# Optimization experiments

Measured on AMD Instinct MI355X. Metric: run time of the kernel, lower is better.

Reference implementation:

```python
import jax, jax.numpy as jnp
import numpy as np

N_NODES = 50000
N_EDGES = 800000
IN_DIM = 128
HID = 256
B_SEEDS = 8192
EPS = 1e-12


def _sage_layer(h, src, dst, Wn, Ws, b):
    # mean-aggregation SAGEConv: fc_self(h) + fc_neigh(mean over in-neighbors)
    msgs = h[src]  # [E, d]
    agg = jax.ops.segment_sum(msgs, dst, num_segments=N_NODES)
    cnt = jax.ops.segment_sum(jnp.ones((src.shape[0], 1), h.dtype), dst, num_segments=N_NODES)
    neigh = agg / jnp.maximum(cnt, 1.0)
    return neigh @ Wn + h @ Ws + b


def _sage(x, src, dst, Wn1, Ws1, b1, Wn2, Ws2, b2):
    h = jax.nn.relu(_sage_layer(x, src, dst, Wn1, Ws1, b1))
    return _sage_layer(h, src, dst, Wn2, Ws2, b2)


def _l2norm(x):
    # F.normalize(p=2, dim=1)
    n = jnp.sqrt(jnp.sum(x * x, axis=1, keepdims=True))
    return x / jnp.maximum(n, EPS)


def _unique_gather(h, ids):
    # torch.unique(ids, return_inverse=True) then h[inverse]
    uniq, inv = jnp.unique(ids, return_inverse=True, size=ids.shape[0], fill_value=0)
    return h[uniq][inv]


def setup_inputs() -> dict:
    key = jax.random.key(0)
    ks = jax.random.split(key, 16)
    s = lambda d: 1.0 / np.sqrt(d)
    return {
        "x_i": jax.random.normal(ks[0], (N_NODES, IN_DIM), jnp.float32),
        "x_j": jax.random.normal(ks[1], (N_NODES, IN_DIM), jnp.float32),
        "src_i": jax.random.randint(ks[2], (N_EDGES,), 0, N_NODES, jnp.int32),
        "dst_i": jax.random.randint(ks[3], (N_EDGES,), 0, N_NODES, jnp.int32),
        "src_j": jax.random.randint(ks[4], (N_EDGES,), 0, N_NODES, jnp.int32),
        "dst_j": jax.random.randint(ks[5], (N_EDGES,), 0, N_NODES, jnp.int32),
        "ids_i": jax.random.randint(ks[6], (B_SEEDS,), 0, N_NODES, jnp.int32),
        "ids_j": jax.random.randint(ks[7], (B_SEEDS,), 0, N_NODES, jnp.int32),
        "Wn1": jax.random.normal(ks[8], (IN_DIM, HID), jnp.float32) * s(IN_DIM),
        "Ws1": jax.random.normal(ks[9], (IN_DIM, HID), jnp.float32) * s(IN_DIM),
        "b1": jnp.zeros((HID,), jnp.float32),
        "Wn2": jax.random.normal(ks[10], (HID, HID), jnp.float32) * s(HID),
        "Ws2": jax.random.normal(ks[11], (HID, HID), jnp.float32) * s(HID),
        "b2": jnp.zeros((HID,), jnp.float32),
        "W_out": jax.random.normal(ks[12], (2 * HID, 1), jnp.float32) * s(2 * HID),
        "b_out": jnp.zeros((1,), jnp.float32),
    }


def reference(x_i, x_j, src_i, dst_i, src_j, dst_j, ids_i, ids_j,
              Wn1, Ws1, b1, Wn2, Ws2, b2, W_out, b_out):
    sage_o_i = _l2norm(_sage(x_i, src_i, dst_i, Wn1, Ws1, b1, Wn2, Ws2, b2))
    sage_o_j = _l2norm(_sage(x_j, src_j, dst_j, Wn1, Ws1, b1, Wn2, Ws2, b2))
    g_i = _unique_gather(sage_o_i, ids_i)  # [B, HID]
    g_j = _unique_gather(sage_o_j, ids_j)
    h_cur = jnp.concatenate([g_i, g_j], axis=-1) @ W_out + b_out  # [B, 1]
    return jnp.stack([h_cur.squeeze(-1)])  # [1, B]
```

## Files before the change

kernel.cpp:

```cpp
#include <hip/hip_runtime.h>

constexpr int NN = 50000;
constexpr int NE = 800000;
constexpr int IND = 128;
constexpr int HD = 256;
constexpr int BS = 8192;
constexpr int NPAD = 50176;
constexpr int NBKT = 196;
constexpr int BCAP = 8192;

typedef __attribute__((ext_vector_type(8))) short short8v;
typedef __attribute__((ext_vector_type(4))) float floatx4;

__device__ inline ushort f2b(float f) {
  unsigned u = __float_as_uint(f);
  unsigned r = (u + 0x7fffu + ((u >> 16) & 1u)) >> 16;
  return (ushort)r;
}
__device__ inline float b2f(ushort b) {
  return __uint_as_float((unsigned)b << 16);
}
__device__ __forceinline__ void acc2(unsigned u, float& a0, float& a1) {
  a0 += __uint_as_float(u << 16);
  a1 += __uint_as_float(u & 0xffff0000u);
}
__device__ inline int wave_incl_scan(int x, int lane) {
#pragma unroll
  for (int d = 1; d < 64; d <<= 1) {
    int y = __shfl_up(x, d);
    if (lane >= d) x += y;
  }
  return x;
}

__device__ __forceinline__ void gload16(const ushort* g, ushort* l) {
  __builtin_amdgcn_global_load_lds(
      (const __attribute__((address_space(1))) void*)g,
      (__attribute__((address_space(3))) void*)l, 16, 0, 0);
}

__global__ __launch_bounds__(256) void k_prep(const float* __restrict__ Wn1,
                                              const float* __restrict__ Ws1,
                                              const float* __restrict__ Wn2,
                                              const float* __restrict__ Ws2,
                                              ushort* __restrict__ Wt,
                                              ushort* __restrict__ Whi,
                                              ushort* __restrict__ Wlo,
                                              int* __restrict__ bcnt) {
  const int b = blockIdx.x, t = threadIdx.x;
  if (b < 256) {
    int i = b * 256 + t;
    int n = i >> 8, k = i & 255;
    float v = (k < 128) ? Wn1[k * HD + n] : Ws1[(k - 128) * HD + n];
    Wt[n * 256 + k] = f2b(v);
  } else if (b < 768) {
    int i = (b - 256) * 256 + t;
    int n = i >> 9, k = i & 511;
    float v = (k < 256) ? Wn2[k * HD + n] : Ws2[(k - 256) * HD + n];
    ushort hi = f2b(v);
    Whi[n * 512 + k] = hi;
    Wlo[n * 512 + k] = f2b(v - b2f(hi));
  } else {
    for (int i = t; i < 2 * NBKT; i += 256) bcnt[i] = 0;
  }
}

__global__ __launch_bounds__(256) void k_bin(const int* __restrict__ src_i,
                                             const int* __restrict__ dst_i,
                                             const int* __restrict__ src_j,
                                             const int* __restrict__ dst_j,
                                             int* __restrict__ bcnt,
                                             int* __restrict__ bucketbuf) {
  __shared__ int hist[NBKT], gbase[NBKT], lcur[NBKT];
  const int blk = blockIdx.x;
  const int g = blk >= 98;
  const int c = blk - g * 98;
  const int* src = g ? src_j : src_i;
  const int* dst = g ? dst_j : dst_i;
  const int t = threadIdx.x;
  if (t < NBKT) hist[t] = 0;
  __syncthreads();
  const int e0 = c * 8192;
#pragma unroll
  for (int k = 0; k < 32; ++k) {
    int e = e0 + k * 256 + t;
    if (e < NE) atomicAdd(&hist[dst[e] >> 8], 1);
  }
  __syncthreads();
  if (t < NBKT) {
    int h = hist[t];
    gbase[t] = h ? atomicAdd(&bcnt[g * NBKT + t], h) : 0;
    lcur[t] = 0;
  }
  __syncthreads();
#pragma unroll
  for (int k = 0; k < 32; ++k) {
    int e = e0 + k * 256 + t;
    if (e < NE) {
      int d = dst[e];
      int b = d >> 8;
      int p = gbase[b] + atomicAdd(&lcur[b], 1);
      if (p < BCAP)
        bucketbuf[(g * NBKT + b) * BCAP + p] = (src[e] << 8) | (d & 255);
    }
  }
}

__global__ __launch_bounds__(256) void k_bktscan(const int* __restrict__ bcnt,
                                                 int* __restrict__ bktbase) {
  __shared__ int wt[4];
  __shared__ int carry, tot;
  const int t = threadIdx.x, lane = t & 63;
  if (t == 0) carry = 0;
  __syncthreads();
  for (int ch = 0; ch < 2; ++ch) {
    int i = ch * 256 + t;
    int v = (i < 2 * NBKT) ? min(bcnt[i], BCAP) : 0;
    int x = wave_incl_scan(v, lane);
    if (lane == 63) wt[t >> 6] = x;
    __syncthreads();
    if (t == 0) {
      int run = 0;
#pragma unroll
      for (int j = 0; j < 4; ++j) { int tv = wt[j]; wt[j] = run; run += tv; }
      tot = run;
    }
    __syncthreads();
    if (i < 2 * NBKT) bktbase[i] = carry + x - v + wt[t >> 6];
    __syncthreads();
    if (t == 0) carry += tot;
    __syncthreads();
  }
}

__global__ __launch_bounds__(256) void k_build(const int* __restrict__ bucketbuf,
                                               const int* __restrict__ bcnt,
                                               const int* __restrict__ bktbase,
                                               int* __restrict__ csr,
                                               int* __restrict__ cnt2,
                                               int* __restrict__ row_start2) {
  __shared__ int hist[256], lstart[256], lcur[256];
  __shared__ int stage[BCAP];
  __shared__ int wt[4];
  const int b = blockIdx.x;
  const int g = b >= NBKT;
  const int bb = b - g * NBKT;
  const int t = threadIdx.x, lane = t & 63;
  const int C = min(bcnt[b], BCAP);
  const int base = bktbase[b];
  const int* buf = bucketbuf + b * BCAP;
  hist[t] = 0;
  __syncthreads();
  for (int i = t; i < C; i += 256) atomicAdd(&hist[buf[i] & 255], 1);
  __syncthreads();
  int v = hist[t];
  int x = wave_incl_scan(v, lane);
  if (lane == 63) wt[t >> 6] = x;
  __syncthreads();
  if (t == 0) {
    int run = 0;
#pragma unroll
    for (int j = 0; j < 4; ++j) { int tv = wt[j]; wt[j] = run; run += tv; }
  }
  __syncthreads();
  int ls = x - v + wt[t >> 6];
  lstart[t] = ls;
  lcur[t] = ls;
  __syncthreads();
  for (int i = t; i < C; i += 256) {
    int val = buf[i];
    int p = atomicAdd(&lcur[val & 255], 1);
    stage[p] = val >> 8;
  }
  __syncthreads();
  for (int i = t; i < C; i += 256) csr[base + i] = stage[i];
  int node = bb * 256 + t;
  cnt2[g * NPAD + node] = v;
  row_start2[g * NPAD + node] = base + ls;
}

__global__ __launch_bounds__(256) void k_tobf16(const float* __restrict__ x_i,
                                                const float* __restrict__ x_j,
                                                ushort* __restrict__ xb2) {
  int i = blockIdx.x * 256 + threadIdx.x;
  int e4 = i * 4;
  int g = e4 >= NN * IND;
  const float* xp = g ? x_j : x_i;
  float4 v = *(const float4*)(xp + (e4 - g * NN * IND));
  ushort4 u;
  u.x = f2b(v.x); u.y = f2b(v.y); u.z = f2b(v.z); u.w = f2b(v.w);
  *(ushort4*)(xb2 + e4) = u;
}

__global__ __launch_bounds__(256) void k_agg1(const ushort* __restrict__ xb2,
                                              const int* __restrict__ csr,
                                              const int* __restrict__ row_start2,
                                              const int* __restrict__ cnt2,
                                              ushort* __restrict__ aggb2) {
  int w = threadIdx.x >> 6, l = threadIdx.x & 63;
  int p = blockIdx.x * 4 + w;
  int nA = p * 2;
  int g = nA >= NN;
  int nl = nA - g * NN;
  int base = g * NPAD + nl;
  int stA = row_start2[base], degA = cnt2[base];
  int stB = row_start2[base + 1], degB = cnt2[base + 1];
  const ushort* xb = xb2 + g * NN * IND;
  float a0A = 0.f, a1A = 0.f, a0B = 0.f, a1B = 0.f;
  int cmn = min(degA, degB);
  int e = 0;
  for (; e + 4 <= cmn; e += 4) {
    int sA0 = csr[stA + e + 0], sA1 = csr[stA + e + 1];
    int sA2 = csr[stA + e + 2], sA3 = csr[stA + e + 3];
    int sB0 = csr[stB + e + 0], sB1 = csr[stB + e + 1];
    int sB2 = csr[stB + e + 2], sB3 = csr[stB + e + 3];
    unsigned uA0 = *(const unsigned*)(xb + sA0 * IND + 2 * l);
    unsigned uA1 = *(const unsigned*)(xb + sA1 * IND + 2 * l);
    unsigned uA2 = *(const unsigned*)(xb + sA2 * IND + 2 * l);
    unsigned uA3 = *(const unsigned*)(xb + sA3 * IND + 2 * l);
    unsigned uB0 = *(const unsigned*)(xb + sB0 * IND + 2 * l);
    unsigned uB1 = *(const unsigned*)(xb + sB1 * IND + 2 * l);
    unsigned uB2 = *(const unsigned*)(xb + sB2 * IND + 2 * l);
    unsigned uB3 = *(const unsigned*)(xb + sB3 * IND + 2 * l);
    acc2(uA0, a0A, a1A); acc2(uA1, a0A, a1A);
    acc2(uA2, a0A, a1A); acc2(uA3, a0A, a1A);
    acc2(uB0, a0B, a1B); acc2(uB1, a0B, a1B);
    acc2(uB2, a0B, a1B); acc2(uB3, a0B, a1B);
  }
  int eA = e, eB = e;
  for (; eA + 4 <= degA; eA += 4) {
    int s0 = csr[stA + eA + 0], s1 = csr[stA + eA + 1];
    int s2 = csr[stA + eA + 2], s3 = csr[stA + eA + 3];
    unsigned u0 = *(const unsigned*)(xb + s0 * IND + 2 * l);
    unsigned u1 = *(const unsigned*)(xb + s1 * IND + 2 * l);
    unsigned u2 = *(const unsigned*)(xb + s2 * IND + 2 * l);
    unsigned u3 = *(const unsigned*)(xb + s3 * IND + 2 * l);
    acc2(u0, a0A, a1A); acc2(u1, a0A, a1A);
    acc2(u2, a0A, a1A); acc2(u3, a0A, a1A);
  }
  for (; eA < degA; ++eA) {
    int s = csr[stA + eA];
    unsigned u = *(const unsigned*)(xb + s * IND + 2 * l);
    acc2(u, a0A, a1A);
  }
  for (; eB + 4 <= degB; eB += 4) {
    int s0 = csr[stB + eB + 0], s1 = csr[stB + eB + 1];
    int s2 = csr[stB + eB + 2], s3 = csr[stB + eB + 3];
    unsigned u0 = *(const unsigned*)(xb + s0 * IND + 2 * l);
    unsigned u1 = *(const unsigned*)(xb + s1 * IND + 2 * l);
    unsigned u2 = *(const unsigned*)(xb + s2 * IND + 2 * l);
    unsigned u3 = *(const unsigned*)(xb + s3 * IND + 2 * l);
    acc2(u0, a0B, a1B); acc2(u1, a0B, a1B);
    acc2(u2, a0B, a1B); acc2(u3, a0B, a1B);
  }
  for (; eB < degB; ++eB) {
    int s = csr[stB + eB];
    unsigned u = *(const unsigned*)(xb + s * IND + 2 * l);
    acc2(u, a0B, a1B);
  }
  float invA = 1.f / (float)max(degA, 1);
  float invB = 1.f / (float)max(degB, 1);
  ushort2 uA, uB;
  uA.x = f2b(a0A * invA); uA.y = f2b(a1A * invA);
  uB.x = f2b(a0B * invB); uB.y = f2b(a1B * invB);
  *(ushort2*)(aggb2 + (g * NN + nl) * IND + 2 * l) = uA;
  *(ushort2*)(aggb2 + (g * NN + nl + 1) * IND + 2 * l) = uB;
}

__global__ __launch_bounds__(256) void k_gemm1(const ushort* __restrict__ aggb2,
                                               const ushort* __restrict__ xb2,
                                               const ushort* __restrict__ Wt,
                                               const float* __restrict__ b1,
                                               ushort* __restrict__ h1b2) {
  __shared__ ushort smem[16384];
  const int t = threadIdx.x;
  const int g = blockIdx.x >= 392;
  const int row0 = (blockIdx.x - g * 392) * 128, col0 = blockIdx.y * 128;
  const ushort* aggb = aggb2 + g * NN * IND;
  const ushort* xb = xb2 + g * NN * IND;
  ushort* h1b = h1b2 + g * NN * HD;
  const int w = t >> 6, l = t & 63;
  const int wm = w & 1, wn = w >> 1;

  const int r0 = t >> 2, cs0 = t & 3;
  const int c0 = cs0 ^ (r0 & 3);
  const int rA0 = min(row0 + r0, NN - 1);
  const int rA1 = min(row0 + r0 + 64, NN - 1);
  const int gA0 = rA0 * IND + c0 * 8;
  const int gA1 = rA1 * IND + c0 * 8;
  const int gB0 = (col0 + r0) * 256 + c0 * 8;
  const int gB1 = (col0 + r0 + 64) * 256 + c0 * 8;
  const int wofs = w * 512;

  floatx4 acc[4][4];
#pragma unroll
  for (int i = 0; i < 4; ++i)
#pragma unroll
    for (int j = 0; j < 4; ++j) acc[i][j] = (floatx4){0.f, 0.f, 0.f, 0.f};

#define STAGE(buf, kk)                                                      \
  do {                                                                      \
    const ushort* Ab = ((kk) < 128) ? (aggb + (kk)) : (xb + ((kk) - 128));  \
    ushort* Ald = smem + (buf) * 4096;                                      \
    ushort* Bld = smem + 8192 + (buf) * 4096;                               \
    gload16(Ab + gA0, Ald + wofs);                                          \
    gload16(Ab + gA1, Ald + 2048 + wofs);                                   \
    gload16(Wt + gB0 + (kk), Bld + wofs);                                   \
    gload16(Wt + gB1 + (kk), Bld + 2048 + wofs);                            \
  } while (0)

  STAGE(0, 0);
  __syncthreads();
  int cur = 0;
  const int rA = l & 15, gg = l >> 4;
  for (int step = 0; step < 8; ++step) {
    if (step < 7) STAGE(cur ^ 1, (step + 1) * 32);
    const ushort* Abuf = smem + cur * 4096;
    const ushort* Bbuf = smem + 8192 + cur * 4096;
    short8v af[4], bf[4];
#pragma unroll
    for (int i = 0; i < 4; ++i) {
      int r = wm * 64 + i * 16 + rA;
      af[i] = *(const short8v*)(Abuf + r * 32 + ((gg ^ (r & 3)) * 8));
    }
#pragma unroll
    for (int j = 0; j < 4; ++j) {
      int r = wn * 64 + j * 16 + rA;
      bf[j] = *(const short8v*)(Bbuf + r * 32 + ((gg ^ (r & 3)) * 8));
    }
#pragma unroll
    for (int i = 0; i < 4; ++i)
#pragma unroll
      for (int j = 0; j < 4; ++j)
        acc[i][j] = __builtin_amdgcn_mfma_f32_16x16x32_bf16(af[i], bf[j],
                                                            acc[i][j], 0, 0, 0);
    if (step < 7) {
      __syncthreads();
      cur ^= 1;
    }
  }
#undef STAGE

  __syncthreads();
  const int rD = l >> 4, cD = l & 15;
#pragma unroll
  for (int j = 0; j < 4; ++j) {
    int cl = wn * 64 + j * 16 + cD;
    float bias = b1[col0 + cl];
#pragma unroll
    for (int i = 0; i < 4; ++i) {
      int rbase = wm * 64 + i * 16 + rD * 4;
#pragma unroll
      for (int rr = 0; rr < 4; ++rr)
        smem[(rbase + rr) * 128 + cl] = f2b(fmaxf(acc[i][j][rr] + bias, 0.f));
    }
  }
  __syncthreads();
  const int rl = t >> 4, ch = t & 15;
#pragma unroll
  for (int it = 0; it < 8; ++it) {
    int row_l = rl + it * 16;
    int grow = row0 + row_l;
    if (grow < NN)
      *(short8v*)(h1b + grow * HD + col0 + ch * 8) =
          *(const short8v*)(smem + row_l * 128 + ch * 8);
  }
}

__global__ __launch_bounds__(256) void k_agg2(
    const ushort* __restrict__ h1b2, const int* __restrict__ csr,
    const int* __restrict__ row_start2, const int* __restrict__ cnt2,
    const int* __restrict__ ids_i, const int* __restrict__ ids_j,
    ushort* __restrict__ A2) {
  __shared__ float red[4][HD];
  const int b = blockIdx.x;
  const int g = b >= BS;
  const int node = (g ? ids_j : ids_i)[b - g * BS];
  const int st = row_start2[g * NPAD + node], deg = cnt2[g * NPAD + node];
  const ushort* h1b = h1b2 + g * NN * HD;
  const int w = threadIdx.x >> 6, l = threadIdx.x & 63;
  float a0 = 0.f, a1 = 0.f, a2 = 0.f, a3 = 0.f;
  int e = w;
  for (; e + 4 < deg; e += 8) {
    int sa = csr[st + e], sb = csr[st + e + 4];
    uint2 ua = *(const uint2*)(h1b + sa * HD + l * 4);
    uint2 ub = *(const uint2*)(h1b + sb * HD + l * 4);
    acc2(ua.x, a0, a1); acc2(ua.y, a2, a3);
    acc2(ub.x, a0, a1); acc2(ub.y, a2, a3);
  }
  if (e < deg) {
    int sa = csr[st + e];
    uint2 ua = *(const uint2*)(h1b + sa * HD + l * 4);
    acc2(ua.x, a0, a1); acc2(ua.y, a2, a3);
  }
  red[w][l * 4 + 0] = a0;
  red[w][l * 4 + 1] = a1;
  red[w][l * 4 + 2] = a2;
  red[w][l * 4 + 3] = a3;
  __syncthreads();
  const int t = threadIdx.x;
  float s = (red[0][t] + red[1][t]) + (red[2][t] + red[3][t]);
  s *= 1.f / (float)max(deg, 1);
  A2[b * 512 + t] = f2b(s);
  A2[b * 512 + 256 + t] = h1b[node * HD + t];
}

__global__ __launch_bounds__(256) void k_head(const ushort* __restrict__ A2,
                                              const ushort* __restrict__ Whi,
                                              const ushort* __restrict__ Wlo,
                                              const float* __restrict__ b2,
                                              const float* __restrict__ W_out,
                                              float* __restrict__ outP) {
  __shared__ ushort Ahl[64 * 32];
  __shared__ ushort Bhl[256 * 32];
  __shared__ ushort Bll[256 * 32];
  __shared__ float sred[4][64][2];
  const int t = threadIdx.x;
  const int row0 = blockIdx.x * 64;
  const int w = t >> 6, l = t & 63;
  const int woff = (row0 >= BS) ? 256 : 0;
  floatx4 acc[4][4];
#pragma unroll
  for (int i = 0; i < 4; ++i)
#pragma unroll
    for (int j = 0; j < 4; ++j) acc[i][j] = (floatx4){0.f, 0.f, 0.f, 0.f};

  for (int kk = 0; kk < 512; kk += 32) {
    {
      int r = t >> 2, c = t & 3;
      int sw = (c ^ (r & 3)) * 8;
      *(short8v*)(Ahl + r * 32 + sw) =
          *(const short8v*)(A2 + (row0 + r) * 512 + kk + c * 8);
    }
#pragma unroll
    for (int s = t; s < 1024; s += 256) {
      int r = s >> 2, c = s & 3;
      int sw = (c ^ (r & 3)) * 8;
      *(short8v*)(Bhl + r * 32 + sw) =
          *(const short8v*)(Whi + r * 512 + kk + c * 8);
      *(short8v*)(Bll + r * 32 + sw) =
          *(const short8v*)(Wlo + r * 512 + kk + c * 8);
    }
    __syncthreads();
    const int rA = l & 15, gg = l >> 4;
    short8v af[4], bh[4], bl[4];
#pragma unroll
    for (int i = 0; i < 4; ++i) {
      int r = i * 16 + rA;
      af[i] = *(const short8v*)(Ahl + r * 32 + ((gg ^ (r & 3)) * 8));
    }
#pragma unroll
    for (int j = 0; j < 4; ++j) {
      int r = w * 64 + j * 16 + rA;
      int sw = (gg ^ (r & 3)) * 8;
      bh[j] = *(const short8v*)(Bhl + r * 32 + sw);
      bl[j] = *(const short8v*)(Bll + r * 32 + sw);
    }
#pragma unroll
    for (int i = 0; i < 4; ++i)
#pragma unroll
      for (int j = 0; j < 4; ++j) {
        acc[i][j] = __builtin_amdgcn_mfma_f32_16x16x32_bf16(af[i], bh[j],
                                                            acc[i][j], 0, 0, 0);
        acc[i][j] = __builtin_amdgcn_mfma_f32_16x16x32_bf16(af[i], bl[j],
                                                            acc[i][j], 0, 0, 0);
      }
    __syncthreads();
  }
  const int cD = l & 15, rD = l >> 4;
  float bj[4], wo[4];
#pragma unroll
  for (int j = 0; j < 4; ++j) {
    int col = w * 64 + j * 16 + cD;
    bj[j] = b2[col];
    wo[j] = W_out[woff + col];
  }
#pragma unroll
  for (int i = 0; i < 4; ++i)
#pragma unroll
    for (int rr = 0; rr < 4; ++rr) {
      float ssv = 0.f, dpv = 0.f;
#pragma unroll
      for (int j = 0; j < 4; ++j) {
        float v = acc[i][j][rr] + bj[j];
        ssv += v * v;
        dpv += v * wo[j];
      }
#pragma unroll
      for (int d = 1; d < 16; d <<= 1) {
        ssv += __shfl_xor(ssv, d);
        dpv += __shfl_xor(dpv, d);
      }
      if (cD == 0) {
        int row = i * 16 + rD * 4 + rr;
        sred[w][row][0] = ssv;
        sred[w][row][1] = dpv;
      }
    }
  __syncthreads();
  if (t < 64) {
    float ss = (sred[0][t][0] + sred[1][t][0]) + (sred[2][t][0] + sred[3][t][0]);
    float dp = (sred[0][t][1] + sred[1][t][1]) + (sred[2][t][1] + sred[3][t][1]);
    outP[row0 + t] = dp / fmaxf(sqrtf(ss), 1e-12f);
  }
}

__global__ __launch_bounds__(256) void k_out2(const float* __restrict__ outP,
                                              const float* __restrict__ b_out,
                                              float* __restrict__ out) {
  int s = blockIdx.x * 256 + threadIdx.x;
  if (s < BS) out[s] = outP[s] + outP[s + BS] + b_out[0];
}

extern "C" void kernel_launch(void* const* d_in, const int* in_sizes, int n_in,
                              void* d_out, int out_size, void* d_ws,
                              size_t ws_size, hipStream_t stream) {
  (void)in_sizes; (void)n_in; (void)out_size; (void)ws_size;
  const float* x_i = (const float*)d_in[0];
  const float* x_j = (const float*)d_in[1];
  const int* src_i = (const int*)d_in[2];
  const int* dst_i = (const int*)d_in[3];
  const int* src_j = (const int*)d_in[4];
  const int* dst_j = (const int*)d_in[5];
  const int* ids_i = (const int*)d_in[6];
  const int* ids_j = (const int*)d_in[7];
  const float* Wn1 = (const float*)d_in[8];
  const float* Ws1 = (const float*)d_in[9];
  const float* b1 = (const float*)d_in[10];
  const float* Wn2 = (const float*)d_in[11];
  const float* Ws2 = (const float*)d_in[12];
  const float* b2 = (const float*)d_in[13];
  const float* W_out = (const float*)d_in[14];
  const float* b_out = (const float*)d_in[15];
  float* out = (float*)d_out;

  char* w = (char*)d_ws;
  int* bcnt       = (int*)(w + 0);
  int* bktbase    = (int*)(w + 2048);
  int* cnt2       = (int*)(w + 4096);
  int* row_start2 = (int*)(w + 405504);
  int* bucketbuf  = (int*)(w + 806912);
  ushort* Wt      = (ushort*)(w + 13651968);
  ushort* W2hi    = (ushort*)(w + 13783040);
  ushort* W2lo    = (ushort*)(w + 14045184);
  ushort* xb2     = (ushort*)(w + 14307328);
  ushort* aggb2   = (ushort*)(w + 39907328);
  ushort* h1b2    = (ushort*)(w + 65507328);
  int* csr        = (int*)(w + 116707328);
  ushort* A2      = (ushort*)(w + 14307328);
  float* outP     = (float*)(w + 31084544);

  k_prep<<<769, 256, 0, stream>>>(Wn1, Ws1, Wn2, Ws2, Wt, W2hi, W2lo, bcnt);
  k_bin<<<196, 256, 0, stream>>>(src_i, dst_i, src_j, dst_j, bcnt, bucketbuf);
  k_bktscan<<<1, 256, 0, stream>>>(bcnt, bktbase);
  k_build<<<392, 256, 0, stream>>>(bucketbuf, bcnt, bktbase, csr, cnt2,
                                   row_start2);
  k_tobf16<<<12500, 256, 0, stream>>>(x_i, x_j, xb2);
  k_agg1<<<12500, 256, 0, stream>>>(xb2, csr, row_start2, cnt2, aggb2);
  k_gemm1<<<dim3(784, 2), 256, 0, stream>>>(aggb2, xb2, Wt, b1, h1b2);
  k_agg2<<<2 * BS, 256, 0, stream>>>(h1b2, csr, row_start2, cnt2, ids_i, ids_j,
                                     A2);
  k_head<<<256, 256, 0, stream>>>(A2, W2hi, W2lo, b2, W_out, outP);
  k_out2<<<32, 256, 0, stream>>>(outP, b_out, out);
}
```

Baseline: 211.8 us.

## Fuse prep, binning and bf16 conversion; fold bucket scan into build; widen gathers

Weight conversion, edge binning and feature bf16 conversion now run as one kernel launch. The bucket counter reset becomes a memset, and the one-block bucket scan is recomputed redundantly inside each build block, so two launches go away. The layer-1 aggregation now uses one wave per node, with half-waves taking alternate edges and 8-byte loads. The layer-2 aggregation uses 16-byte loads with half-wave splitting and shuffle reductions. The aim is lower launch overhead and better memory-level parallelism, at the cost of the same scan being repeated in every build block.

```diff
diff --git a/kernel.cpp b/kernel.cpp
--- a/kernel.cpp
+++ b/kernel.cpp
@@ -39,45 +39,49 @@
       (__attribute__((address_space(3))) void*)l, 16, 0, 0);
 }
 
-__global__ __launch_bounds__(256) void k_prep(const float* __restrict__ Wn1,
-                                              const float* __restrict__ Ws1,
-                                              const float* __restrict__ Wn2,
-                                              const float* __restrict__ Ws2,
-                                              ushort* __restrict__ Wt,
-                                              ushort* __restrict__ Whi,
-                                              ushort* __restrict__ Wlo,
-                                              int* __restrict__ bcnt) {
+__global__ __launch_bounds__(256) void k_bin_cvt(
+    const float* __restrict__ Wn1, const float* __restrict__ Ws1,
+    const float* __restrict__ Wn2, const float* __restrict__ Ws2,
+    ushort* __restrict__ Wt, ushort* __restrict__ Whi,
+    ushort* __restrict__ Wlo, const int* __restrict__ src_i,
+    const int* __restrict__ dst_i, const int* __restrict__ src_j,
+    const int* __restrict__ dst_j, int* __restrict__ bcnt,
+    int* __restrict__ bucketbuf, const float* __restrict__ x_i,
+    const float* __restrict__ x_j, ushort* __restrict__ xb2) {
+  __shared__ int hist[NBKT], gbase[NBKT], lcur[NBKT];
   const int b = blockIdx.x, t = threadIdx.x;
   if (b < 256) {
     int i = b * 256 + t;
     int n = i >> 8, k = i & 255;
     float v = (k < 128) ? Wn1[k * HD + n] : Ws1[(k - 128) * HD + n];
     Wt[n * 256 + k] = f2b(v);
-  } else if (b < 768) {
+    return;
+  }
+  if (b < 768) {
     int i = (b - 256) * 256 + t;
     int n = i >> 9, k = i & 511;
     float v = (k < 256) ? Wn2[k * HD + n] : Ws2[(k - 256) * HD + n];
     ushort hi = f2b(v);
     Whi[n * 512 + k] = hi;
     Wlo[n * 512 + k] = f2b(v - b2f(hi));
-  } else {
-    for (int i = t; i < 2 * NBKT; i += 256) bcnt[i] = 0;
-  }
-}
-
-__global__ __launch_bounds__(256) void k_bin(const int* __restrict__ src_i,
-                                             const int* __restrict__ dst_i,
-                                             const int* __restrict__ src_j,
-                                             const int* __restrict__ dst_j,
-                                             int* __restrict__ bcnt,
-                                             int* __restrict__ bucketbuf) {
-  __shared__ int hist[NBKT], gbase[NBKT], lcur[NBKT];
-  const int blk = blockIdx.x;
+    return;
+  }
+  if (b >= 964) {
+    int i = (b - 964) * 256 + t;
+    int e4 = i * 4;
+    int g = e4 >= NN * IND;
+    const float* xp = g ? x_j : x_i;
+    float4 v = *(const float4*)(xp + (e4 - g * NN * IND));
+    ushort4 u;
+    u.x = f2b(v.x); u.y = f2b(v.y); u.z = f2b(v.z); u.w = f2b(v.w);
+    *(ushort4*)(xb2 + e4) = u;
+    return;
+  }
+  const int blk = b - 768;
   const int g = blk >= 98;
   const int c = blk - g * 98;
   const int* src = g ? src_j : src_i;
   const int* dst = g ? dst_j : dst_i;
-  const int t = threadIdx.x;
   if (t < NBKT) hist[t] = 0;
   __syncthreads();
   const int e0 = c * 8192;
@@ -98,18 +102,26 @@
     int e = e0 + k * 256 + t;
     if (e < NE) {
       int d = dst[e];
-      int b = d >> 8;
-      int p = gbase[b] + atomicAdd(&lcur[b], 1);
+      int bk = d >> 8;
+      int p = gbase[bk] + atomicAdd(&lcur[bk], 1);
       if (p < BCAP)
-        bucketbuf[(g * NBKT + b) * BCAP + p] = (src[e] << 8) | (d & 255);
-    }
-  }
-}
-
-__global__ __launch_bounds__(256) void k_bktscan(const int* __restrict__ bcnt,
-                                                 int* __restrict__ bktbase) {
-  __shared__ int wt[4];
-  __shared__ int carry, tot;
+        bucketbuf[(g * NBKT + bk) * BCAP + p] = (src[e] << 8) | (d & 255);
+    }
+  }
+}
+
+__global__ __launch_bounds__(256) void k_build(const int* __restrict__ bucketbuf,
+                                               const int* __restrict__ bcnt,
+                                               int* __restrict__ csr,
+                                               int* __restrict__ cnt2,
+                                               int* __restrict__ row_start2) {
+  __shared__ int hist[256], lcur[256];
+  __shared__ int stage[BCAP];
+  __shared__ int wtv[4];
+  __shared__ int carry, tot, baseSh;
+  const int b = blockIdx.x;
+  const int g = b >= NBKT;
+  const int bb = b - g * NBKT;
   const int t = threadIdx.x, lane = t & 63;
   if (t == 0) carry = 0;
   __syncthreads();
@@ -117,37 +129,22 @@
     int i = ch * 256 + t;
     int v = (i < 2 * NBKT) ? min(bcnt[i], BCAP) : 0;
     int x = wave_incl_scan(v, lane);
-    if (lane == 63) wt[t >> 6] = x;
+    if (lane == 63) wtv[t >> 6] = x;
     __syncthreads();
     if (t == 0) {
       int run = 0;
 #pragma unroll
-      for (int j = 0; j < 4; ++j) { int tv = wt[j]; wt[j] = run; run += tv; }
+      for (int j = 0; j < 4; ++j) { int tv = wtv[j]; wtv[j] = run; run += tv; }
       tot = run;
     }
     __syncthreads();
-    if (i < 2 * NBKT) bktbase[i] = carry + x - v + wt[t >> 6];
+    if (i == b) baseSh = carry + x - v + wtv[t >> 6];
     __syncthreads();
     if (t == 0) carry += tot;
     __syncthreads();
   }
-}
-
-__global__ __launch_bounds__(256) void k_build(const int* __restrict__ bucketbuf,
-                                               const int* __restrict__ bcnt,
-                                               const int* __restrict__ bktbase,
-                                               int* __restrict__ csr,
-                                               int* __restrict__ cnt2,
-                                               int* __restrict__ row_start2) {
-  __shared__ int hist[256], lstart[256], lcur[256];
-  __shared__ int stage[BCAP];
-  __shared__ int wt[4];
-  const int b = blockIdx.x;
-  const int g = b >= NBKT;
-  const int bb = b - g * NBKT;
-  const int t = threadIdx.x, lane = t & 63;
+  const int base = baseSh;
   const int C = min(bcnt[b], BCAP);
-  const int base = bktbase[b];
   const int* buf = bucketbuf + b * BCAP;
   hist[t] = 0;
   __syncthreads();
@@ -155,16 +152,15 @@
   __syncthreads();
   int v = hist[t];
   int x = wave_incl_scan(v, lane);
-  if (lane == 63) wt[t >> 6] = x;
+  if (lane == 63) wtv[t >> 6] = x;
   __syncthreads();
   if (t == 0) {
     int run = 0;
 #pragma unroll
-    for (int j = 0; j < 4; ++j) { int tv = wt[j]; wt[j] = run; run += tv; }
-  }
-  __syncthreads();
-  int ls = x - v + wt[t >> 6];
-  lstart[t] = ls;
+    for (int j = 0; j < 4; ++j) { int tv = wtv[j]; wtv[j] = run; run += tv; }
+  }
+  __syncthreads();
+  int ls = x - v + wtv[t >> 6];
   lcur[t] = ls;
   __syncthreads();
   for (int i = t; i < C; i += 256) {
@@ -177,19 +173,6 @@
   int node = bb * 256 + t;
   cnt2[g * NPAD + node] = v;
   row_start2[g * NPAD + node] = base + ls;
-}
-
-__global__ __launch_bounds__(256) void k_tobf16(const float* __restrict__ x_i,
-                                                const float* __restrict__ x_j,
-                                                ushort* __restrict__ xb2) {
-  int i = blockIdx.x * 256 + threadIdx.x;
-  int e4 = i * 4;
-  int g = e4 >= NN * IND;
-  const float* xp = g ? x_j : x_i;
-  float4 v = *(const float4*)(xp + (e4 - g * NN * IND));
-  ushort4 u;
-  u.x = f2b(v.x); u.y = f2b(v.y); u.z = f2b(v.z); u.w = f2b(v.w);
-  *(ushort4*)(xb2 + e4) = u;
 }
 
 __global__ __launch_bounds__(256) void k_agg1(const ushort* __restrict__ xb2,
@@ -198,73 +181,49 @@
                                               const int* __restrict__ cnt2,
                                               ushort* __restrict__ aggb2) {
   int w = threadIdx.x >> 6, l = threadIdx.x & 63;
-  int p = blockIdx.x * 4 + w;
-  int nA = p * 2;
-  int g = nA >= NN;
-  int nl = nA - g * NN;
-  int base = g * NPAD + nl;
-  int stA = row_start2[base], degA = cnt2[base];
-  int stB = row_start2[base + 1], degB = cnt2[base + 1];
+  int n = blockIdx.x * 4 + w;
+  int g = n >= NN;
+  int nl = n - g * NN;
+  int st = row_start2[g * NPAD + nl], deg = cnt2[g * NPAD + nl];
   const ushort* xb = xb2 + g * NN * IND;
-  float a0A = 0.f, a1A = 0.f, a0B = 0.f, a1B = 0.f;
-  int cmn = min(degA, degB);
+  const int h = l >> 5, c = l & 31;
+  float a0 = 0.f, a1 = 0.f, a2 = 0.f, a3 = 0.f;
   int e = 0;
-  for (; e + 4 <= cmn; e += 4) {
-    int sA0 = csr[stA + e + 0], sA1 = csr[stA + e + 1];
-    int sA2 = csr[stA + e + 2], sA3 = csr[stA + e + 3];
-    int sB0 = csr[stB + e + 0], sB1 = csr[stB + e + 1];
-    int sB2 = csr[stB + e + 2], sB3 = csr[stB + e + 3];
-    unsigned uA0 = *(const unsigned*)(xb + sA0 * IND + 2 * l);
-    unsigned uA1 = *(const unsigned*)(xb + sA1 * IND + 2 * l);
-    unsigned uA2 = *(const unsigned*)(xb + sA2 * IND + 2 * l);
-    unsigned uA3 = *(const unsigned*)(xb + sA3 * IND + 2 * l);
-    unsigned uB0 = *(const unsigned*)(xb + sB0 * IND + 2 * l);
-    unsigned uB1 = *(const unsigned*)(xb + sB1 * IND + 2 * l);
-    unsigned uB2 = *(const unsigned*)(xb + sB2 * IND + 2 * l);
-    unsigned uB3 = *(const unsigned*)(xb + sB3 * IND + 2 * l);
-    acc2(uA0, a0A, a1A); acc2(uA1, a0A, a1A);
-    acc2(uA2, a0A, a1A); acc2(uA3, a0A, a1A);
-    acc2(uB0, a0B, a1B); acc2(uB1, a0B, a1B);
-    acc2(uB2, a0B, a1B); acc2(uB3, a0B, a1B);
-  }
-  int eA = e, eB = e;
-  for (; eA + 4 <= degA; eA += 4) {
-    int s0 = csr[stA + eA + 0], s1 = csr[stA + eA + 1];
-    int s2 = csr[stA + eA + 2], s3 = csr[stA + eA + 3];
-    unsigned u0 = *(const unsigned*)(xb + s0 * IND + 2 * l);
-    unsigned u1 = *(const unsigned*)(xb + s1 * IND + 2 * l);
-    unsigned u2 = *(const unsigned*)(xb + s2 * IND + 2 * l);
-    unsigned u3 = *(const unsigned*)(xb + s3 * IND + 2 * l);
-    acc2(u0, a0A, a1A); acc2(u1, a0A, a1A);
-    acc2(u2, a0A, a1A); acc2(u3, a0A, a1A);
-  }
-  for (; eA < degA; ++eA) {
-    int s = csr[stA + eA];
-    unsigned u = *(const unsigned*)(xb + s * IND + 2 * l);
-    acc2(u, a0A, a1A);
-  }
-  for (; eB + 4 <= degB; eB += 4) {
-    int s0 = csr[stB + eB + 0], s1 = csr[stB + eB + 1];
-    int s2 = csr[stB + eB + 2], s3 = csr[stB + eB + 3];
-    unsigned u0 = *(const unsigned*)(xb + s0 * IND + 2 * l);
-    unsigned u1 = *(const unsigned*)(xb + s1 * IND + 2 * l);
-    unsigned u2 = *(const unsigned*)(xb + s2 * IND + 2 * l);
-    unsigned u3 = *(const unsigned*)(xb + s3 * IND + 2 * l);
-    acc2(u0, a0B, a1B); acc2(u1, a0B, a1B);
-    acc2(u2, a0B, a1B); acc2(u3, a0B, a1B);
-  }
-  for (; eB < degB; ++eB) {
-    int s = csr[stB + eB];
-    unsigned u = *(const unsigned*)(xb + s * IND + 2 * l);
-    acc2(u, a0B, a1B);
-  }
-  float invA = 1.f / (float)max(degA, 1);
-  float invB = 1.f / (float)max(degB, 1);
-  ushort2 uA, uB;
-  uA.x = f2b(a0A * invA); uA.y = f2b(a1A * invA);
-  uB.x = f2b(a0B * invB); uB.y = f2b(a1B * invB);
-  *(ushort2*)(aggb2 + (g * NN + nl) * IND + 2 * l) = uA;
-  *(ushort2*)(aggb2 + (g * NN + nl + 1) * IND + 2 * l) = uB;
+  for (; e + 8 <= deg; e += 8) {
+    int s0 = csr[st + e + 0 + h];
+    int s1 = csr[st + e + 2 + h];
+    int s2 = csr[st + e + 4 + h];
+    int s3 = csr[st + e + 6 + h];
+    uint2 u0 = *(const uint2*)(xb + s0 * IND + c * 4);
+    uint2 u1 = *(const uint2*)(xb + s1 * IND + c * 4);
+    uint2 u2 = *(const uint2*)(xb + s2 * IND + c * 4);
+    uint2 u3 = *(const uint2*)(xb + s3 * IND + c * 4);
+    acc2(u0.x, a0, a1); acc2(u0.y, a2, a3);
+    acc2(u1.x, a0, a1); acc2(u1.y, a2, a3);
+    acc2(u2.x, a0, a1); acc2(u2.y, a2, a3);
+    acc2(u3.x, a0, a1); acc2(u3.y, a2, a3);
+  }
+  for (; e + 2 <= deg; e += 2) {
+    int s = csr[st + e + h];
+    uint2 u = *(const uint2*)(xb + s * IND + c * 4);
+    acc2(u.x, a0, a1); acc2(u.y, a2, a3);
+  }
+  if (e < deg && h == 0) {
+    int s = csr[st + e];
+    uint2 u = *(const uint2*)(xb + s * IND + c * 4);
+    acc2(u.x, a0, a1); acc2(u.y, a2, a3);
+  }
+  a0 += __shfl_xor(a0, 32);
+  a1 += __shfl_xor(a1, 32);
+  a2 += __shfl_xor(a2, 32);
+  a3 += __shfl_xor(a3, 32);
+  if (h == 0) {
+    float inv = 1.f / (float)max(deg, 1);
+    ushort4 u;
+    u.x = f2b(a0 * inv); u.y = f2b(a1 * inv);
+    u.z = f2b(a2 * inv); u.w = f2b(a3 * inv);
+    *(ushort4*)(aggb2 + (g * NN + nl) * IND + c * 4) = u;
+  }
 }
 
 __global__ __launch_bounds__(256) void k_gemm1(const ushort* __restrict__ aggb2,
@@ -379,24 +338,33 @@
   const int st = row_start2[g * NPAD + node], deg = cnt2[g * NPAD + node];
   const ushort* h1b = h1b2 + g * NN * HD;
   const int w = threadIdx.x >> 6, l = threadIdx.x & 63;
+  const int h = l >> 5, c = l & 31;
   float a0 = 0.f, a1 = 0.f, a2 = 0.f, a3 = 0.f;
-  int e = w;
-  for (; e + 4 < deg; e += 8) {
-    int sa = csr[st + e], sb = csr[st + e + 4];
-    uint2 ua = *(const uint2*)(h1b + sa * HD + l * 4);
-    uint2 ub = *(const uint2*)(h1b + sb * HD + l * 4);
-    acc2(ua.x, a0, a1); acc2(ua.y, a2, a3);
-    acc2(ub.x, a0, a1); acc2(ub.y, a2, a3);
+  float a4 = 0.f, a5 = 0.f, a6 = 0.f, a7 = 0.f;
+  int e = w * 2 + h;
+  for (; e + 8 < deg; e += 16) {
+    int s0 = csr[st + e], s1 = csr[st + e + 8];
+    uint4 u0 = *(const uint4*)(h1b + s0 * HD + c * 8);
+    uint4 u1 = *(const uint4*)(h1b + s1 * HD + c * 8);
+    acc2(u0.x, a0, a1); acc2(u0.y, a2, a3);
+    acc2(u0.z, a4, a5); acc2(u0.w, a6, a7);
+    acc2(u1.x, a0, a1); acc2(u1.y, a2, a3);
+    acc2(u1.z, a4, a5); acc2(u1.w, a6, a7);
   }
   if (e < deg) {
-    int sa = csr[st + e];
-    uint2 ua = *(const uint2*)(h1b + sa * HD + l * 4);
-    acc2(ua.x, a0, a1); acc2(ua.y, a2, a3);
-  }
-  red[w][l * 4 + 0] = a0;
-  red[w][l * 4 + 1] = a1;
-  red[w][l * 4 + 2] = a2;
-  red[w][l * 4 + 3] = a3;
+    int s = csr[st + e];
+    uint4 u = *(const uint4*)(h1b + s * HD + c * 8);
+    acc2(u.x, a0, a1); acc2(u.y, a2, a3);
+    acc2(u.z, a4, a5); acc2(u.w, a6, a7);
+  }
+  a0 += __shfl_xor(a0, 32); a1 += __shfl_xor(a1, 32);
+  a2 += __shfl_xor(a2, 32); a3 += __shfl_xor(a3, 32);
+  a4 += __shfl_xor(a4, 32); a5 += __shfl_xor(a5, 32);
+  a6 += __shfl_xor(a6, 32); a7 += __shfl_xor(a7, 32);
+  if (h == 0) {
+    *(float4*)&red[w][c * 8] = (float4){a0, a1, a2, a3};
+    *(float4*)&red[w][c * 8 + 4] = (float4){a4, a5, a6, a7};
+  }
   __syncthreads();
   const int t = threadIdx.x;
   float s = (red[0][t] + red[1][t]) + (red[2][t] + red[3][t]);
@@ -536,7 +504,6 @@
 
   char* w = (char*)d_ws;
   int* bcnt       = (int*)(w + 0);
-  int* bktbase    = (int*)(w + 2048);
   int* cnt2       = (int*)(w + 4096);
   int* row_start2 = (int*)(w + 405504);
   int* bucketbuf  = (int*)(w + 806912);
@@ -550,13 +517,12 @@
   ushort* A2      = (ushort*)(w + 14307328);
   float* outP     = (float*)(w + 31084544);
 
-  k_prep<<<769, 256, 0, stream>>>(Wn1, Ws1, Wn2, Ws2, Wt, W2hi, W2lo, bcnt);
-  k_bin<<<196, 256, 0, stream>>>(src_i, dst_i, src_j, dst_j, bcnt, bucketbuf);
-  k_bktscan<<<1, 256, 0, stream>>>(bcnt, bktbase);
-  k_build<<<392, 256, 0, stream>>>(bucketbuf, bcnt, bktbase, csr, cnt2,
-                                   row_start2);
-  k_tobf16<<<12500, 256, 0, stream>>>(x_i, x_j, xb2);
-  k_agg1<<<12500, 256, 0, stream>>>(xb2, csr, row_start2, cnt2, aggb2);
+  hipMemsetAsync(bcnt, 0, 2 * NBKT * sizeof(int), stream);
+  k_bin_cvt<<<13464, 256, 0, stream>>>(Wn1, Ws1, Wn2, Ws2, Wt, W2hi, W2lo,
+                                       src_i, dst_i, src_j, dst_j, bcnt,
+                                       bucketbuf, x_i, x_j, xb2);
+  k_build<<<392, 256, 0, stream>>>(bucketbuf, bcnt, csr, cnt2, row_start2);
+  k_agg1<<<25000, 256, 0, stream>>>(xb2, csr, row_start2, cnt2, aggb2);
   k_gemm1<<<dim3(784, 2), 256, 0, stream>>>(aggb2, xb2, Wt, b1, h1b2);
   k_agg2<<<2 * BS, 256, 0, stream>>>(h1b2, csr, row_start2, cnt2, ids_i, ids_j,
                                      A2);
```

After: 201.8 us. 4.7% less time.
